# Kernel tuning notes

Hardware: AMD Instinct MI355X
Metric: run time of the kernel (lower is better)

The kernel has to match this reference:

```python
import jax, jax.numpy as jnp
import numpy as np

B, T, C, H = 2, 2048, 1024, 16
HD = C // H  # head dim = 64


def setup_inputs() -> dict:
    key = jax.random.key(0)
    k1, k2, k3 = jax.random.split(key, 3)
    scale = 0.02
    x = jax.random.normal(k1, (B, T, C), dtype=jnp.float32)
    w_attn = jax.random.normal(k2, (C, 3 * C), dtype=jnp.float32) * scale
    b_attn = jnp.zeros((3 * C,), dtype=jnp.float32)
    w_proj = jax.random.normal(k3, (C, C), dtype=jnp.float32) * scale
    b_proj = jnp.zeros((C,), dtype=jnp.float32)
    return {"x": x, "w_attn": w_attn, "b_attn": b_attn, "w_proj": w_proj, "b_proj": b_proj}


def reference(x, w_attn, b_attn, w_proj, b_proj):
    b, t, c = x.shape
    qkv = x @ w_attn + b_attn  # [B,T,3C]
    q, k, v = jnp.split(qkv, 3, axis=-1)
    # [B,T,C] -> [B,H,T,HD]
    q = q.reshape(b, t, H, HD).transpose(0, 2, 1, 3)
    k = k.reshape(b, t, H, HD).transpose(0, 2, 1, 3)
    v = v.reshape(b, t, H, HD).transpose(0, 2, 1, 3)
    att = jnp.einsum('bhqd,bhkd->bhqk', q, k) * (1.0 / jnp.sqrt(jnp.float32(HD)))
    causal = jnp.tril(jnp.ones((t, t), dtype=bool))  # [T,T]
    att = jnp.where(causal[None, None, :, :], att, jnp.float32(-jnp.inf))
    att = jax.nn.softmax(att, axis=-1)
    y = jnp.einsum('bhqk,bhkd->bhqd', att, v)
    y = y.transpose(0, 2, 1, 3).reshape(b, t, c)
    return y @ w_proj + b_proj
```

## Files before the change

### kernel.cpp

```cpp
#include <hip/hip_runtime.h>


typedef unsigned short u16;
typedef unsigned short u16x8 __attribute__((ext_vector_type(8)));
typedef __bf16 bf16x8 __attribute__((ext_vector_type(8)));
typedef __bf16 bf16x4 __attribute__((ext_vector_type(4)));
typedef float f32x4 __attribute__((ext_vector_type(4)));

#define MFMA16(a, b, c) __builtin_amdgcn_mfma_f32_16x16x32_bf16(a, b, c, 0, 0, 0)

static __device__ __forceinline__ u16 f2b(float f) {
  union { float f; unsigned int i; } x; x.f = f;
  unsigned int r = x.i + 0x7fffu + ((x.i >> 16) & 1u);
  return (u16)(r >> 16);
}
static __device__ __forceinline__ float b2f(u16 u) {
  union { unsigned int i; float f; } x; x.i = ((unsigned int)u) << 16; return x.f;
}

static __device__ __forceinline__ void gload_lds16(const u16* g, u16* l) {
#if defined(__HIP_DEVICE_COMPILE__)
  __builtin_amdgcn_global_load_lds(
      (const __attribute__((address_space(1))) unsigned int*)g,
      (__attribute__((address_space(3))) unsigned int*)l,
      16, 0, 0);
#else
  (void)g; (void)l;
#endif
}

__global__ __launch_bounds__(256) void cast_f32_bf16(
    const float* __restrict__ in, u16* __restrict__ out) {
  int i = (blockIdx.x * 256 + threadIdx.x) * 8;
  float4 a = *(const float4*)&in[i];
  float4 b = *(const float4*)&in[i + 4];
  u16x8 o;
  o[0] = f2b(a.x); o[1] = f2b(a.y); o[2] = f2b(a.z); o[3] = f2b(a.w);
  o[4] = f2b(b.x); o[5] = f2b(b.y); o[6] = f2b(b.z); o[7] = f2b(b.w);
  *(u16x8*)&out[i] = o;
}

__global__ __launch_bounds__(256) void transpose_f32_bf16(
    const float* __restrict__ in, u16* __restrict__ out, int R, int Cc) {
  __shared__ u16 tile[32][33];
  int bx = blockIdx.x, by = blockIdx.y;
  int tx = threadIdx.x, ty = threadIdx.y;
#pragma unroll
  for (int i = 0; i < 4; i++) {
    int r = by * 32 + ty + i * 8;
    int c = bx * 32 + tx;
    tile[ty + i * 8][tx] = f2b(in[r * Cc + c]);
  }
  __syncthreads();
#pragma unroll
  for (int i = 0; i < 4; i++) {
    int r = bx * 32 + ty + i * 8;
    int c = by * 32 + tx;
    out[r * R + c] = tile[tx][ty + i * 8];
  }
}

__global__ __launch_bounds__(256) void transpose_v(
    const u16* __restrict__ in, u16* __restrict__ out) {
  int bh = blockIdx.y;
  int t = blockIdx.x * 128 + (threadIdx.x & 127);
  int dg = (threadIdx.x >> 7) * 32;
  const u16* src = in + (bh * 2048 + t) * 64;
  u16* dst = out + bh * 64 * 2048 + t;
#pragma unroll
  for (int i = 0; i < 32; i++) {
    int d = dg + i;
    dst[d * 2048] = src[d];
  }
}

template <int MODE>
__global__ __launch_bounds__(256, 2) void gemm_bt(
    const u16* __restrict__ A, const u16* __restrict__ Bt,
    const float* __restrict__ bias, float* __restrict__ out,
    u16* __restrict__ Qb, u16* __restrict__ Kb, u16* __restrict__ Vb,
    int M, int N, int K) {
  __shared__ u16 lA[128 * 32];
  __shared__ u16 lB[128 * 32];

  const int tid = threadIdx.x;
  const int lane = tid & 63;
  const int w = tid >> 6;
  const int wm = (w >> 1) * 64, wn = (w & 1) * 64;
  const int l15 = lane & 15, quad = lane >> 4;
  const int m0 = blockIdx.y * 128, n0 = blockIdx.x * 128;

  const int srow = lane >> 2;
  const int scol = (lane & 3) * 8;

  f32x4 acc[4][4] = {};

  for (int k0 = 0; k0 < K; k0 += 32) {
    __syncthreads();
#pragma unroll
    for (int h = 0; h < 2; h++) {
      int r = h * 64 + w * 16 + srow;
      gload_lds16(&A[(m0 + r) * K + k0 + scol], &lA[h * 2048 + w * 512 + lane * 8]);
      gload_lds16(&Bt[(n0 + r) * K + k0 + scol], &lB[h * 2048 + w * 512 + lane * 8]);
    }
    __syncthreads();

    bf16x8 af[4], bfr[4];
#pragma unroll
    for (int mi = 0; mi < 4; mi++)
      af[mi] = *(const bf16x8*)&lA[(wm + mi * 16 + l15) * 32 + quad * 8];
#pragma unroll
    for (int ni = 0; ni < 4; ni++)
      bfr[ni] = *(const bf16x8*)&lB[(wn + ni * 16 + l15) * 32 + quad * 8];
#pragma unroll
    for (int mi = 0; mi < 4; mi++)
#pragma unroll
      for (int ni = 0; ni < 4; ni++)
        acc[mi][ni] = MFMA16(af[mi], bfr[ni], acc[mi][ni]);
  }

#pragma unroll
  for (int mi = 0; mi < 4; mi++) {
#pragma unroll
    for (int ni = 0; ni < 4; ni++) {
      int n = n0 + wn + ni * 16 + l15;
      float bv = bias[n];
#pragma unroll
      for (int reg = 0; reg < 4; reg++) {
        int m = m0 + wm + mi * 16 + quad * 4 + reg;
        float v = acc[mi][ni][reg] + bv;
        if (MODE == 1) {
          out[m * N + n] = v;
        } else {
          int which = n >> 10;
          if (which == 1) v *= 0.18033688011112042f;
          int hn = n & 1023;
          int hh = hn >> 6, d = hn & 63;
          int b = m >> 11, t = m & 2047;
          u16* dst = (which == 0) ? Qb : ((which == 1) ? Kb : Vb);
          dst[(((b << 4) + hh) * 2048 + t) * 64 + d] = f2b(v);
        }
      }
    }
  }
}

__global__ __launch_bounds__(256, 4) void attn_split(
    const u16* __restrict__ Qg, const u16* __restrict__ Kg,
    const u16* __restrict__ Vt, u16* __restrict__ Yg,
    u16* __restrict__ Opart, float* __restrict__ lpart) {
  __shared__ u16 lk[64 * 72];
  __shared__ u16 lvt[64 * 72];

  const int x = 39 - blockIdx.x;
  const int bh = blockIdx.y;
  int p, s, ns;
  if (x < 4)       { p = x;          s = 0;           ns = 1; }
  else if (x < 12) { int r = x - 4;  p = 4 + (r >> 1);  s = r & 1;  ns = 2; }
  else if (x < 24) { int r = x - 12; p = 8 + r / 3;     s = r % 3;  ns = 3; }
  else             { int r = x - 24; p = 12 + (r >> 2); s = r & 3;  ns = 4; }
  const int kts = s * 8;
  const int ktotal = 2 * p + 2;
  const int kend = (kts + 8 < ktotal) ? (kts + 8) : ktotal;
  const int qtA = 2 * p;

  const int tid = threadIdx.x;
  const int lane = tid & 63;
  const int w = tid >> 6;
  const int l15 = lane & 15, quad = lane >> 4;
  const int base = bh * 2048 * 64;
  const int vbase = bh * 64 * 2048;

  const int sr = tid >> 3;
  const int sc = (tid & 7) * 8;

  const u16* qrA = Qg + base + (qtA * 64 + w * 16 + l15) * 64;
  bf16x8 bq0A = *(const bf16x8*)&qrA[quad * 8];
  bf16x8 bq1A = *(const bf16x8*)&qrA[32 + quad * 8];
  const u16* qrB = qrA + 64 * 64;
  bf16x8 bq0B = *(const bf16x8*)&qrB[quad * 8];
  bf16x8 bq1B = *(const bf16x8*)&qrB[32 + quad * 8];

  const int qgA = qtA * 64 + w * 16 + l15;

  u16x8 onesu = {0x3F80, 0x3F80, 0x3F80, 0x3F80, 0x3F80, 0x3F80, 0x3F80, 0x3F80};
  bf16x8 ones = *(const bf16x8*)&onesu;

  const u16* kp = Kg + base;
  const u16* vp = Vt + vbase;

  u16x8 kr[2], vr[2];
  {
    int kvb = kts * 64;
#pragma unroll
    for (int h = 0; h < 2; h++) {
      int r = sr + h * 32;
      kr[h] = *(const u16x8*)&kp[(kvb + r) * 64 + sc];
      vr[h] = *(const u16x8*)&vp[r * 2048 + kvb + sc];
    }
  }

  f32x4 oA[4] = {}, oB[4] = {};
  f32x4 lA4 = {}, lB4 = {};

  for (int kt = kts; kt < kend; kt++) {
    __syncthreads();
#pragma unroll
    for (int h = 0; h < 2; h++) {
      int r = sr + h * 32;
      *(u16x8*)&lk[r * 72 + sc] = kr[h];
      *(u16x8*)&lvt[r * 72 + sc] = vr[h];
    }
    __syncthreads();
    if (kt + 1 < kend) {
      int kvb = (kt + 1) * 64;
#pragma unroll
      for (int h = 0; h < 2; h++) {
        int r = sr + h * 32;
        kr[h] = *(const u16x8*)&kp[(kvb + r) * 64 + sc];
        vr[h] = *(const u16x8*)&vp[r * 2048 + kvb + sc];
      }
    }

    const bool mA = (kt >= qtA);
    const bool mB = (kt == qtA + 1);

#pragma unroll
    for (int u = 0; u < 2; u++) {
      bf16x8 paA, paB;
#pragma unroll
      for (int half = 0; half < 2; half++) {
        int nt = 2 * u + half;
        bf16x8 ak0 = *(const bf16x8*)&lk[(nt * 16 + l15) * 72 + quad * 8];
        bf16x8 ak1 = *(const bf16x8*)&lk[(nt * 16 + l15) * 72 + 32 + quad * 8];
        f32x4 stA = {};
        stA = MFMA16(ak0, bq0A, stA);
        stA = MFMA16(ak1, bq1A, stA);
        f32x4 stB = {};
        stB = MFMA16(ak0, bq0B, stB);
        stB = MFMA16(ak1, bq1B, stB);
        int kv0 = kt * 64 + nt * 16 + quad * 4;
#pragma unroll
        for (int reg = 0; reg < 4; reg++) {
          int kv = kv0 + reg;
          float svA = stA[reg];
          if (mA && kv > qgA) svA = -1e30f;
          float svB = stB[reg];
          if (mB && kv > qgA + 64) svB = -1e30f;
          paA[half * 4 + reg] = (__bf16)exp2f(svA);
          paB[half * 4 + reg] = (__bf16)exp2f(svB);
        }
      }
      lA4 = MFMA16(paA, ones, lA4);
      lB4 = MFMA16(paB, ones, lB4);
#pragma unroll
      for (int dt = 0; dt < 4; dt++) {
        const u16* vrow = &lvt[(dt * 16 + l15) * 72 + u * 32 + quad * 4];
        bf16x4 lo = *(const bf16x4*)&vrow[0];
        bf16x4 hi = *(const bf16x4*)&vrow[16];
        bf16x8 bv;
#pragma unroll
        for (int j = 0; j < 4; j++) { bv[j] = lo[j]; bv[4 + j] = hi[j]; }
        oA[dt] = MFMA16(paA, bv, oA[dt]);
        oB[dt] = MFMA16(paB, bv, oB[dt]);
      }
    }
  }

  if (ns == 1) {
    const int b = bh >> 4, hh = bh & 15;
    float invA[4], invB[4];
#pragma unroll
    for (int reg = 0; reg < 4; reg++) {
      invA[reg] = 1.0f / lA4[reg];
      invB[reg] = 1.0f / lB4[reg];
    }
#pragma unroll
    for (int dt = 0; dt < 4; dt++)
#pragma unroll
      for (int reg = 0; reg < 4; reg++) {
        int qA = qtA * 64 + w * 16 + quad * 4 + reg;
        int col = hh * 64 + dt * 16 + l15;
        Yg[(b * 2048 + qA) * 1024 + col] = f2b(oA[dt][reg] * invA[reg]);
        Yg[(b * 2048 + qA + 64) * 1024 + col] = f2b(oB[dt][reg] * invB[reg]);
      }
  } else {
    const int pidx = bh * 40 + x;
    u16* op = Opart + pidx * 8192;
#pragma unroll
    for (int dt = 0; dt < 4; dt++)
#pragma unroll
      for (int reg = 0; reg < 4; reg++) {
        int rA = w * 16 + quad * 4 + reg;
        op[rA * 64 + dt * 16 + l15] = f2b(oA[dt][reg]);
        op[(rA + 64) * 64 + dt * 16 + l15] = f2b(oB[dt][reg]);
      }
    if (l15 == 0) {
#pragma unroll
      for (int reg = 0; reg < 4; reg++) {
        int rA = w * 16 + quad * 4 + reg;
        lpart[pidx * 128 + rA] = lA4[reg];
        lpart[pidx * 128 + rA + 64] = lB4[reg];
      }
    }
  }
}

__global__ __launch_bounds__(256) void attn_combine(
    const u16* __restrict__ Opart, const float* __restrict__ lpart,
    u16* __restrict__ Yg) {
  const int pp = 4 + blockIdx.x;
  const int bh = blockIdx.y;
  const int tid = threadIdx.x;
  const int row = tid >> 1;
  const int cg = (tid & 1) * 32;
  int xb, ns;
  if (pp < 8)       { xb = 4  + (pp - 4) * 2;  ns = 2; }
  else if (pp < 12) { xb = 12 + (pp - 8) * 3;  ns = 3; }
  else              { xb = 24 + (pp - 12) * 4; ns = 4; }

  float acc[32] = {};
  float lsum = 0.f;
  for (int i = 0; i < ns; i++) {
    int pidx = bh * 40 + xb + i;
    lsum += lpart[pidx * 128 + row];
    const u16* oprow = Opart + pidx * 8192 + row * 64 + cg;
#pragma unroll
    for (int v = 0; v < 4; v++) {
      u16x8 a = *(const u16x8*)&oprow[v * 8];
#pragma unroll
      for (int j = 0; j < 8; j++) acc[v * 8 + j] += b2f(a[j]);
    }
  }
  float inv = 1.0f / lsum;
  const int b = bh >> 4, hh = bh & 15;
  u16* y = Yg + ((long)(b * 2048 + pp * 128 + row)) * 1024 + hh * 64 + cg;
#pragma unroll
  for (int v = 0; v < 4; v++) {
    u16x8 o;
#pragma unroll
    for (int j = 0; j < 8; j++) o[j] = f2b(acc[v * 8 + j] * inv);
    *(u16x8*)&y[v * 8] = o;
  }
}

__global__ __launch_bounds__(256, 4) void attn_kernel(
    const u16* __restrict__ Qg, const u16* __restrict__ Kg,
    const u16* __restrict__ Vt, u16* __restrict__ Yg) {
  __shared__ u16 lk[64 * 72];
  __shared__ u16 lvt[64 * 72];

  const int qt = 31 - blockIdx.x;
  const int bh = blockIdx.y;
  const int tid = threadIdx.x;
  const int lane = tid & 63;
  const int w = tid >> 6;
  const int l15 = lane & 15, quad = lane >> 4;
  const int qbase = qt * 64;
  const int base = bh * 2048 * 64;
  const int vbase = bh * 64 * 2048;
  const int sr = tid >> 3;
  const int sc = (tid & 7) * 8;

  const u16* qrow = Qg + base + (qbase + w * 16 + l15) * 64;
  bf16x8 bq0 = *(const bf16x8*)&qrow[quad * 8];
  bf16x8 bq1 = *(const bf16x8*)&qrow[32 + quad * 8];

  u16x8 onesu = {0x3F80, 0x3F80, 0x3F80, 0x3F80, 0x3F80, 0x3F80, 0x3F80, 0x3F80};
  bf16x8 ones = *(const bf16x8*)&onesu;

  const u16* kp = Kg + base;
  const u16* vp = Vt + vbase;

  u16x8 kr[2], vr[2];
#pragma unroll
  for (int h = 0; h < 2; h++) {
    int r = sr + h * 32;
    kr[h] = *(const u16x8*)&kp[r * 64 + sc];
    vr[h] = *(const u16x8*)&vp[r * 2048 + sc];
  }

  f32x4 oacc[4] = {};
  f32x4 lacc = {};

  for (int kt = 0; kt <= qt; kt++) {
    __syncthreads();
#pragma unroll
    for (int h = 0; h < 2; h++) {
      int r = sr + h * 32;
      *(u16x8*)&lk[r * 72 + sc] = kr[h];
      *(u16x8*)&lvt[r * 72 + sc] = vr[h];
    }
    __syncthreads();
    if (kt < qt) {
      int kvb = (kt + 1) * 64;
#pragma unroll
      for (int h = 0; h < 2; h++) {
        int r = sr + h * 32;
        kr[h] = *(const u16x8*)&kp[(kvb + r) * 64 + sc];
        vr[h] = *(const u16x8*)&vp[r * 2048 + kvb + sc];
      }
    }

    const bool diag = (kt == qt);
    const int qloc = w * 16 + l15;
#pragma unroll
    for (int u = 0; u < 2; u++) {
      bf16x8 pa;
#pragma unroll
      for (int half = 0; half < 2; half++) {
        int nt = 2 * u + half;
        bf16x8 ak0 = *(const bf16x8*)&lk[(nt * 16 + l15) * 72 + quad * 8];
        bf16x8 ak1 = *(const bf16x8*)&lk[(nt * 16 + l15) * 72 + 32 + quad * 8];
        f32x4 st = {};
        st = MFMA16(ak0, bq0, st);
        st = MFMA16(ak1, bq1, st);
#pragma unroll
        for (int reg = 0; reg < 4; reg++) {
          float sv = st[reg];
          if (diag && (nt * 16 + quad * 4 + reg) > qloc) sv = -1e30f;
          pa[half * 4 + reg] = (__bf16)exp2f(sv);
        }
      }
      lacc = MFMA16(pa, ones, lacc);
#pragma unroll
      for (int dt = 0; dt < 4; dt++) {
        const u16* vrow = &lvt[(dt * 16 + l15) * 72 + u * 32 + quad * 4];
        bf16x4 lo = *(const bf16x4*)&vrow[0];
        bf16x4 hi = *(const bf16x4*)&vrow[16];
        bf16x8 bv;
#pragma unroll
        for (int j = 0; j < 4; j++) { bv[j] = lo[j]; bv[4 + j] = hi[j]; }
        oacc[dt] = MFMA16(pa, bv, oacc[dt]);
      }
    }
  }

  const int b = bh >> 4, hh = bh & 15;
  float inv[4];
#pragma unroll
  for (int reg = 0; reg < 4; reg++) inv[reg] = 1.0f / lacc[reg];
#pragma unroll
  for (int dt = 0; dt < 4; dt++)
#pragma unroll
    for (int reg = 0; reg < 4; reg++) {
      int q = qbase + w * 16 + quad * 4 + reg;
      int col = hh * 64 + dt * 16 + l15;
      Yg[(b * 2048 + q) * 1024 + col] = f2b(oacc[dt][reg] * inv[reg]);
    }
}

extern "C" void kernel_launch(void* const* d_in, const int* in_sizes, int n_in,
                              void* d_out, int out_size, void* d_ws, size_t ws_size,
                              hipStream_t stream) {
  const float* x      = (const float*)d_in[0];
  const float* w_attn = (const float*)d_in[1];
  const float* b_attn = (const float*)d_in[2];
  const float* w_proj = (const float*)d_in[3];
  const float* b_proj = (const float*)d_in[4];
  float* out = (float*)d_out;

  char* ws = (char*)d_ws;
  u16* wattnT = (u16*)(ws);
  u16* wprojT = (u16*)(ws + 6291456);
  u16* xb     = (u16*)(ws + 8388608);
  u16* Vt     = xb;
  u16* Qb     = (u16*)(ws + 16777216);
  u16* Kb     = (u16*)(ws + 25165824);
  u16* Vb     = (u16*)(ws + 33554432);
  u16* Yb     = (u16*)(ws + 41943040);
  u16* Opart  = (u16*)(ws + 50331648);
  float* lpart = (float*)(ws + 71303168);

  const bool split = (ws_size >= 71958528ULL);

  cast_f32_bf16<<<2048, 256, 0, stream>>>(x, xb);
  transpose_f32_bf16<<<dim3(96, 32), dim3(32, 8), 0, stream>>>(w_attn, wattnT, 1024, 3072);
  transpose_f32_bf16<<<dim3(32, 32), dim3(32, 8), 0, stream>>>(w_proj, wprojT, 1024, 1024);
  gemm_bt<0><<<dim3(24, 32), 256, 0, stream>>>(xb, wattnT, b_attn, nullptr,
                                               Qb, Kb, Vb, 4096, 3072, 1024);
  transpose_v<<<dim3(16, 32), 256, 0, stream>>>(Vb, Vt);
  if (split) {
    attn_split<<<dim3(40, 32), 256, 0, stream>>>(Qb, Kb, Vt, Yb, Opart, lpart);
    attn_combine<<<dim3(12, 32), 256, 0, stream>>>(Opart, lpart, Yb);
  } else {
    attn_kernel<<<dim3(32, 32), 256, 0, stream>>>(Qb, Kb, Vt, Yb);
  }
  gemm_bt<1><<<dim3(8, 32), 256, 0, stream>>>(Yb, wprojT, b_proj, out,
                                              nullptr, nullptr, nullptr, 4096, 1024, 1024);
}
```

Before: 201.1 us.

## Balance attention KV splits, specialize masked tiles, raise GEMM occupancy

Attention splits now divide the KV tiles evenly across the ns splits instead of fixed chunks of 8, so splits carry similar work. The inner loop is specialized into three paths: unmasked tiles with no mask checks, the diagonal tile that masks only query tile A, and the last tile that skips query tile A entirely since it is fully masked. This removes per-element mask branches and wasted MFMA/exp work on the final tile. The GEMM launch bound also moves from 2 to 3 waves per SIMD, which may constrain registers and cause spills. Code size grows because the loop body now appears three times.

```diff
diff --git a/kernel.cpp b/kernel.cpp
--- a/kernel.cpp
+++ b/kernel.cpp
@@ -75,7 +75,7 @@
 }
 
 template <int MODE>
-__global__ __launch_bounds__(256, 2) void gemm_bt(
+__global__ __launch_bounds__(256, 3) void gemm_bt(
     const u16* __restrict__ A, const u16* __restrict__ Bt,
     const float* __restrict__ bias, float* __restrict__ out,
     u16* __restrict__ Qb, u16* __restrict__ Kb, u16* __restrict__ Vb,
@@ -159,9 +159,10 @@
   else if (x < 12) { int r = x - 4;  p = 4 + (r >> 1);  s = r & 1;  ns = 2; }
   else if (x < 24) { int r = x - 12; p = 8 + r / 3;     s = r % 3;  ns = 3; }
   else             { int r = x - 24; p = 12 + (r >> 2); s = r & 3;  ns = 4; }
-  const int kts = s * 8;
   const int ktotal = 2 * p + 2;
-  const int kend = (kts + 8 < ktotal) ? (kts + 8) : ktotal;
+  const int lb = ktotal / ns, rem = ktotal % ns;
+  const int kts = s * lb + ((s < rem) ? s : rem);
+  const int kend = kts + lb + (s < rem ? 1 : 0);
   const int qtA = 2 * p;
 
   const int tid = threadIdx.x;
@@ -181,7 +182,7 @@
   bf16x8 bq0B = *(const bf16x8*)&qrB[quad * 8];
   bf16x8 bq1B = *(const bf16x8*)&qrB[32 + quad * 8];
 
-  const int qgA = qtA * 64 + w * 16 + l15;
+  const int qlocal = w * 16 + l15;
 
   u16x8 onesu = {0x3F80, 0x3F80, 0x3F80, 0x3F80, 0x3F80, 0x3F80, 0x3F80, 0x3F80};
   bf16x8 ones = *(const bf16x8*)&onesu;
@@ -222,47 +223,108 @@
       }
     }
 
-    const bool mA = (kt >= qtA);
-    const bool mB = (kt == qtA + 1);
-
-#pragma unroll
-    for (int u = 0; u < 2; u++) {
-      bf16x8 paA, paB;
-#pragma unroll
-      for (int half = 0; half < 2; half++) {
-        int nt = 2 * u + half;
-        bf16x8 ak0 = *(const bf16x8*)&lk[(nt * 16 + l15) * 72 + quad * 8];
-        bf16x8 ak1 = *(const bf16x8*)&lk[(nt * 16 + l15) * 72 + 32 + quad * 8];
-        f32x4 stA = {};
-        stA = MFMA16(ak0, bq0A, stA);
-        stA = MFMA16(ak1, bq1A, stA);
-        f32x4 stB = {};
-        stB = MFMA16(ak0, bq0B, stB);
-        stB = MFMA16(ak1, bq1B, stB);
-        int kv0 = kt * 64 + nt * 16 + quad * 4;
-#pragma unroll
-        for (int reg = 0; reg < 4; reg++) {
-          int kv = kv0 + reg;
-          float svA = stA[reg];
-          if (mA && kv > qgA) svA = -1e30f;
-          float svB = stB[reg];
-          if (mB && kv > qgA + 64) svB = -1e30f;
-          paA[half * 4 + reg] = (__bf16)exp2f(svA);
-          paB[half * 4 + reg] = (__bf16)exp2f(svB);
-        }
-      }
-      lA4 = MFMA16(paA, ones, lA4);
-      lB4 = MFMA16(paB, ones, lB4);
-#pragma unroll
-      for (int dt = 0; dt < 4; dt++) {
-        const u16* vrow = &lvt[(dt * 16 + l15) * 72 + u * 32 + quad * 4];
-        bf16x4 lo = *(const bf16x4*)&vrow[0];
-        bf16x4 hi = *(const bf16x4*)&vrow[16];
-        bf16x8 bv;
-#pragma unroll
-        for (int j = 0; j < 4; j++) { bv[j] = lo[j]; bv[4 + j] = hi[j]; }
-        oA[dt] = MFMA16(paA, bv, oA[dt]);
-        oB[dt] = MFMA16(paB, bv, oB[dt]);
+    if (kt < qtA) {
+#pragma unroll
+      for (int u = 0; u < 2; u++) {
+        bf16x8 paA, paB;
+#pragma unroll
+        for (int half = 0; half < 2; half++) {
+          int nt = 2 * u + half;
+          bf16x8 ak0 = *(const bf16x8*)&lk[(nt * 16 + l15) * 72 + quad * 8];
+          bf16x8 ak1 = *(const bf16x8*)&lk[(nt * 16 + l15) * 72 + 32 + quad * 8];
+          f32x4 stA = {};
+          stA = MFMA16(ak0, bq0A, stA);
+          stA = MFMA16(ak1, bq1A, stA);
+          f32x4 stB = {};
+          stB = MFMA16(ak0, bq0B, stB);
+          stB = MFMA16(ak1, bq1B, stB);
+#pragma unroll
+          for (int reg = 0; reg < 4; reg++) {
+            paA[half * 4 + reg] = (__bf16)exp2f(stA[reg]);
+            paB[half * 4 + reg] = (__bf16)exp2f(stB[reg]);
+          }
+        }
+        lA4 = MFMA16(paA, ones, lA4);
+        lB4 = MFMA16(paB, ones, lB4);
+#pragma unroll
+        for (int dt = 0; dt < 4; dt++) {
+          const u16* vrow = &lvt[(dt * 16 + l15) * 72 + u * 32 + quad * 4];
+          bf16x4 lo = *(const bf16x4*)&vrow[0];
+          bf16x4 hi = *(const bf16x4*)&vrow[16];
+          bf16x8 bv;
+#pragma unroll
+          for (int j = 0; j < 4; j++) { bv[j] = lo[j]; bv[4 + j] = hi[j]; }
+          oA[dt] = MFMA16(paA, bv, oA[dt]);
+          oB[dt] = MFMA16(paB, bv, oB[dt]);
+        }
+      }
+    } else if (kt == qtA) {
+#pragma unroll
+      for (int u = 0; u < 2; u++) {
+        bf16x8 paA, paB;
+#pragma unroll
+        for (int half = 0; half < 2; half++) {
+          int nt = 2 * u + half;
+          bf16x8 ak0 = *(const bf16x8*)&lk[(nt * 16 + l15) * 72 + quad * 8];
+          bf16x8 ak1 = *(const bf16x8*)&lk[(nt * 16 + l15) * 72 + 32 + quad * 8];
+          f32x4 stA = {};
+          stA = MFMA16(ak0, bq0A, stA);
+          stA = MFMA16(ak1, bq1A, stA);
+          f32x4 stB = {};
+          stB = MFMA16(ak0, bq0B, stB);
+          stB = MFMA16(ak1, bq1B, stB);
+          int loc0 = nt * 16 + quad * 4;
+#pragma unroll
+          for (int reg = 0; reg < 4; reg++) {
+            float svA = (loc0 + reg > qlocal) ? -1e30f : stA[reg];
+            paA[half * 4 + reg] = (__bf16)exp2f(svA);
+            paB[half * 4 + reg] = (__bf16)exp2f(stB[reg]);
+          }
+        }
+        lA4 = MFMA16(paA, ones, lA4);
+        lB4 = MFMA16(paB, ones, lB4);
+#pragma unroll
+        for (int dt = 0; dt < 4; dt++) {
+          const u16* vrow = &lvt[(dt * 16 + l15) * 72 + u * 32 + quad * 4];
+          bf16x4 lo = *(const bf16x4*)&vrow[0];
+          bf16x4 hi = *(const bf16x4*)&vrow[16];
+          bf16x8 bv;
+#pragma unroll
+          for (int j = 0; j < 4; j++) { bv[j] = lo[j]; bv[4 + j] = hi[j]; }
+          oA[dt] = MFMA16(paA, bv, oA[dt]);
+          oB[dt] = MFMA16(paB, bv, oB[dt]);
+        }
+      }
+    } else {
+#pragma unroll
+      for (int u = 0; u < 2; u++) {
+        bf16x8 paB;
+#pragma unroll
+        for (int half = 0; half < 2; half++) {
+          int nt = 2 * u + half;
+          bf16x8 ak0 = *(const bf16x8*)&lk[(nt * 16 + l15) * 72 + quad * 8];
+          bf16x8 ak1 = *(const bf16x8*)&lk[(nt * 16 + l15) * 72 + 32 + quad * 8];
+          f32x4 stB = {};
+          stB = MFMA16(ak0, bq0B, stB);
+          stB = MFMA16(ak1, bq1B, stB);
+          int loc0 = nt * 16 + quad * 4;
+#pragma unroll
+          for (int reg = 0; reg < 4; reg++) {
+            float svB = (loc0 + reg > qlocal) ? -1e30f : stB[reg];
+            paB[half * 4 + reg] = (__bf16)exp2f(svB);
+          }
+        }
+        lB4 = MFMA16(paB, ones, lB4);
+#pragma unroll
+        for (int dt = 0; dt < 4; dt++) {
+          const u16* vrow = &lvt[(dt * 16 + l15) * 72 + u * 32 + quad * 4];
+          bf16x4 lo = *(const bf16x4*)&vrow[0];
+          bf16x4 hi = *(const bf16x4*)&vrow[16];
+          bf16x8 bv;
+#pragma unroll
+          for (int j = 0; j < 4; j++) { bv[j] = lo[j]; bv[4 + j] = hi[j]; }
+          oB[dt] = MFMA16(paB, bv, oB[dt]);
+        }
       }
     }
   }
```

Measured after the change: 214.3 us. 1.07x slower.
